# Optimization experiments

Measured on AMD Instinct MI355X. Metric: run time of the kernel, lower is better.

The kernel has to match this reference:

```python
import jax, jax.numpy as jnp
import numpy as np
from jax import lax

H = 1024
W = 1024
WIN = 32
STR = 16
NH = (H - WIN) // STR + 1  # 63
N = NH * NH                # 3969 patches
DN3 = ('NCDHW', 'OIDHW', 'NCDHW')
DN2 = ('NCHW', 'OIHW', 'NCHW')


def setup_inputs() -> dict:
    key = jax.random.key(0)
    ks = jax.random.split(key, 13)
    r = lambda k, s, sc=0.05: jax.random.normal(k, s, dtype=jnp.float32) * sc
    return {
        'x1': jax.random.normal(ks[0], (1, 1, 1, H, W), jnp.float32),
        'x2': jax.random.normal(ks[1], (1, 1, 1, H, W), jnp.float32),
        'conv1_w': r(ks[2], (24, 1, 2, 8, 8)),      # Conv3d(1,24,(2,8,8)) [O,I,D,H,W]
        'conv1_b': r(ks[3], (24,)),
        'conv2_w': r(ks[4], (60, 24, 5, 5)),         # Conv2d(24,60,5)
        'conv2_b': r(ks[5], (60,)),
        'deconv2_w': r(ks[6], (60, 24, 5, 5)),       # ConvTranspose2d(60,24,5) [I,O,kH,kW]
        'deconv2_b': r(ks[7], (24,)),
        'deconv1_w': r(ks[8], (24, 1, 2, 8, 8)),     # ConvTranspose3d(24,1,(2,8,8)) [I,O,D,H,W]
        'deconv1_b': r(ks[9], (1,)),
        'lin_w': r(ks[10], (N, 2), 0.5),             # per-patch Linear(2,1) weights
        'lin_b': r(ks[11], (N,), 0.5),               # per-patch Linear(2,1) bias
        'linear1_w': r(ks[12], (1, 1), 0.5),         # Linear(1,1,bias=False)
    }


def _conv(x, w, b, dn):
    nd = w.ndim - 2
    y = lax.conv_general_dilated(x, w, (1,) * nd, 'VALID', dimension_numbers=dn)
    return y + b.reshape((1, -1) + (1,) * nd)


def _convT(x, w, b, dn):
    # stride-1, pad-0 transposed conv == full-pad conv with flipped, IO-swapped kernel
    nd = w.ndim - 2
    wf = jnp.flip(w, axis=tuple(range(2, w.ndim))).swapaxes(0, 1)  # [O,I,*k]
    pad = [(k - 1, k - 1) for k in w.shape[2:]]
    y = lax.conv_general_dilated(x, wf, (1,) * nd, pad, dimension_numbers=dn)
    return y + b.reshape((1, -1) + (1,) * nd)


def reference(x1, x2, conv1_w, conv1_b, conv2_w, conv2_b, deconv2_w, deconv2_b,
              deconv1_w, deconv1_b, lin_w, lin_b, linear1_w):
    x = jnp.concatenate([x1, x2], axis=2)[0, 0]  # [2,H,W]
    idx = (jnp.arange(NH) * STR)[:, None] + jnp.arange(WIN)[None, :]  # [NH,32]
    # unfold dims 3,4 with window 32 / stride 16 -> [2,NH,NW,32,32]
    patches = x[:, idx[:, None, :, None], idx[None, :, None, :]]
    outX = patches.reshape(2, N, WIN, WIN).transpose(1, 0, 2, 3)[:, None]  # [N,1,2,32,32]
    h = jax.nn.elu(_conv(outX, conv1_w, conv1_b, DN3))        # [N,24,1,25,25]
    h = jax.nn.relu(_conv(h[:, :, 0], conv2_w, conv2_b, DN2))  # [N,60,21,21]
    h = jax.nn.elu(_convT(h, deconv2_w, deconv2_b, DN2))       # [N,24,25,25]
    h = _convT(h[:, :, None], deconv1_w, deconv1_b, DN3)       # [N,1,2,32,32]
    # per-patch Linear(2,1) over depth channels, batched over all patches
    p = jnp.einsum('nchw,nc->nhw', h[:, 0], lin_w) + lin_b[:, None, None]  # [N,32,32]
    p = p.reshape(NH, NH, WIN, WIN)
    # col2im: overlap-add fold, block 32, stride 16 -> [H,W]
    recon = jnp.zeros((H, W), jnp.float32).at[idx[:, None, :, None], idx[None, :, None, :]].add(p)
    outX2 = recon * linear1_w[0, 0]  # Linear(1,1,bias=False) per pixel
    return x2 - outX2.reshape(x2.shape)
```

## Files before the change

kernel.cpp:

```cpp
#include <hip/hip_runtime.h>
#include <hip/hip_bf16.h>

static constexpr int H_ = 1024;
static constexpr int W_ = 1024;
static constexpr int STR_ = 16;
static constexpr int NH_ = 63;
static constexpr int NPATCH_ = NH_ * NH_;
static constexpr int NGRP_ = 32;
static constexpr int NBLK_ = NH_ * NGRP_;

typedef short bf16x8 __attribute__((ext_vector_type(8)));
typedef short short4v __attribute__((ext_vector_type(4)));
typedef float f32x4 __attribute__((ext_vector_type(4)));

static constexpr int GAP16   = 49200;
static constexpr int CP0     = 49216;
static constexpr int CP1     = 55360;
static constexpr int SH2_0   = 49216;
static constexpr int SH2SZ   = 52920;
static constexpr int SH2_1   = SH2_0 + SH2SZ;
static constexpr int ZROW    = 155056;
static constexpr int H3SZ    = 30000;
static constexpr int SWC0    = 60000;
static constexpr int SWC1    = 64096;
static constexpr int SPA     = 68192;
static constexpr int LDS_BYTES = 155200;

__device__ __forceinline__ unsigned short f2bf(float x) {
    __hip_bfloat16 b = __float2bfloat16(x);
    return __builtin_bit_cast(unsigned short, b);
}

__device__ __forceinline__ f32x4 mfma_bf16(bf16x8 a, bf16x8 b, f32x4 c) {
    return __builtin_amdgcn_mfma_f32_16x16x32_bf16(a, b, c, 0, 0, 0);
}

__device__ __forceinline__ float elu_neg(float x) { return __expf(x) - 1.f; }

__global__
__attribute__((amdgpu_flat_work_group_size(1024, 1024), amdgpu_waves_per_eu(4, 4)))
void fused_patch_kernel(
    const float* __restrict__ x1, const float* __restrict__ x2,
    const float* __restrict__ c1b, const float* __restrict__ c2b,
    const float* __restrict__ d2b, const float* __restrict__ d1b,
    const float* __restrict__ lin_w, const float* __restrict__ lin_b,
    const unsigned short* __restrict__ w1frag,
    const unsigned short* __restrict__ w2frag,
    const unsigned short* __restrict__ dw2frag,
    const float* __restrict__ dw1,
    float* __restrict__ recon)
{
    __shared__ alignas(16) char sbuf[LDS_BYTES];
    const int b   = blockIdx.x;
    const int pi  = b / NGRP_, g = b - pi * NGRP_;
    const int pj0 = 2 * g;
    const int npat = (pj0 + 1 < NH_) ? 2 : 1;
    const int n0  = pi * NH_ + pj0;
    const int n1  = (npat == 2) ? (n0 + 1) : n0;
    const int Y0  = pi * STR_, X0 = pj0 * STR_;
    const int t   = (int)threadIdx.x;
    const int wv  = t >> 6, lane = t & 63;
    const int ln15 = lane & 15, quad = lane >> 4;

    bf16x8 w1b[8];
    #pragma unroll
    for (int gg = 0; gg < 8; ++gg)
        w1b[gg] = *(const bf16x8*)(w1frag + (gg * 64 + lane) * 8);
    const float lw00 = lin_w[2 * n0], lw01 = lin_w[2 * n0 + 1];
    const float lw10 = lin_w[2 * n1], lw11 = lin_w[2 * n1 + 1];
    const float lbn0 = lin_b[n0], lbn1 = lin_b[n1];
    const float d1b0 = d1b[0];
    const f32x4 c1bq0 = *(const f32x4*)(c1b + quad * 4);
    f32x4 c1bq1 = (f32x4){0.f, 0.f, 0.f, 0.f};
    if (quad < 2) c1bq1 = *(const f32x4*)(c1b + 16 + quad * 4);
    const f32x4 d2bq0 = *(const f32x4*)(d2b + quad * 4);
    f32x4 d2bq1 = (f32x4){0.f, 0.f, 0.f, 0.f};
    if (quad < 2) d2bq1 = *(const f32x4*)(d2b + 16 + quad * 4);
    float dwp[4] = {0.f, 0.f, 0.f, 0.f};
    {
        int r0 = t >> 5, c0 = t & 31;
        if (c0 < 24) {
            dwp[0] = dw1[(c0 * 2 + 0) * 64 + r0];
            dwp[1] = dw1[(c0 * 2 + 1) * 64 + r0];
        }
        int k1 = t + 1024, r1 = k1 >> 5, c1 = k1 & 31;
        if (c1 < 24) {
            dwp[2] = dw1[(c1 * 2 + 0) * 64 + r1];
            dwp[3] = dw1[(c1 * 2 + 1) * 64 + r1];
        }
    }

    if (t < 4)       ((float*)(sbuf + GAP16))[t] = 0.f;
    else if (t < 8)  ((float*)(sbuf + SH2_1))[t - 4] = 0.f;
    else if (t < 42) ((float*)(sbuf + ZROW))[t - 8] = 0.f;
    #pragma unroll
    for (int it = 0; it < 3; ++it) {
        int k = t + it * 1024;
        int d = (k >= 1536) ? 1 : 0;
        int rem = k - d * 1536;
        int y = rem / 48, x = rem - y * 48;
        int xg = X0 + x; if (xg > W_ - 1) xg = W_ - 1;
        unsigned short bb = f2bf((d ? x2 : x1)[(Y0 + y) * W_ + xg]);
        int row = (d * 32 + y) * 48;
        ((unsigned short*)(sbuf + CP0))[row + x] = bb;
        if (x > 0) ((unsigned short*)(sbuf + CP1))[row + x - 1] = bb;
    }
    __syncthreads();

    for (int tl = wv; tl < 65; tl += 16) {
        const int rawm = tl * 16 + ln15;
        int m = rawm; if (m > 1024) m = 1024;
        int u = m / 41, v = m - u * 41;
        const char* cps = sbuf + ((v & 1) ? CP1 : CP0);
        const int vb2 = (v & ~1) * 2;
        f32x4 acc[2];
        acc[0] = (f32x4){0.f, 0.f, 0.f, 0.f};
        acc[1] = (f32x4){0.f, 0.f, 0.f, 0.f};
        #pragma unroll
        for (int kc = 0; kc < 4; ++kc) {
            const int idx8 = kc * 4 + quad;
            const int dd = idx8 >> 3, pp = idx8 & 7;
            const unsigned int* ap = (const unsigned int*)(cps + (dd * 32 + u + pp) * 96 + vb2);
            union { unsigned int u4[4]; bf16x8 v8; } af;
            af.u4[0] = ap[0]; af.u4[1] = ap[1]; af.u4[2] = ap[2]; af.u4[3] = ap[3];
            acc[0] = mfma_bf16(w1b[kc * 2 + 0], af.v8, acc[0]);
            acc[1] = mfma_bf16(w1b[kc * 2 + 1], af.v8, acc[1]);
        }
        if (rawm < 1025) {
            char* rowp = sbuf + rawm * 48;
            short4v p0;
            #pragma unroll
            for (int r = 0; r < 4; ++r) {
                float hv = acc[0][r] + c1bq0[r];
                hv = hv > 0.f ? hv : elu_neg(hv);
                p0[r] = (short)f2bf(hv);
            }
            *(short4v*)(rowp + quad * 8) = p0;
            if (quad < 2) {
                short4v p1;
                #pragma unroll
                for (int r = 0; r < 4; ++r) {
                    float hw = acc[1][r] + c1bq1[r];
                    hw = hw > 0.f ? hw : elu_neg(hw);
                    p1[r] = (short)f2bf(hw);
                }
                *(short4v*)(rowp + 32 + quad * 8) = p1;
            }
        }
    }
    __syncthreads();

    auto s2pass = [&](int t0, int t1) {
        const bool h1 = (t1 < 56);
        int ab[2], loc[2], Pp[2];
        #pragma unroll
        for (int i = 0; i < 2; ++i) {
            int tt = i ? (h1 ? t1 : t0) : t0;
            int P = (tt >= 28) ? 1 : 0;
            int lc = tt - P * 28;
            int mm = lc * 16 + ln15; if (mm > 440) mm = 440;
            int y = mm / 21, x = mm - y * 21;
            ab[i] = (y * 41 + P * 16 + x) * 48;
            loc[i] = lc; Pp[i] = P;
        }
        f32x4 acc2[2][4];
        #pragma unroll
        for (int i = 0; i < 2; ++i)
            #pragma unroll
            for (int nt = 0; nt < 4; ++nt)
                acc2[i][nt] = (f32x4){0.f, 0.f, 0.f, 0.f};
        const unsigned short* wb = w2frag + lane * 8;
        #pragma unroll
        for (int p = 0; p < 5; ++p) {
            #pragma unroll
            for (int q = 0; q < 5; ++q) {
                const int tap  = p * 5 + q;
                const int toff = (p * 41 + q) * 48;
                bf16x8 bfr[4];
                #pragma unroll
                for (int nt = 0; nt < 4; ++nt)
                    bfr[nt] = *(const bf16x8*)(wb + (tap * 4 + nt) * 512);
                {
                    bf16x8 a = *(const bf16x8*)(sbuf + ab[0] + toff + quad * 16);
                    #pragma unroll
                    for (int nt = 0; nt < 4; ++nt)
                        acc2[0][nt] = mfma_bf16(bfr[nt], a, acc2[0][nt]);
                }
                if (h1) {
                    bf16x8 a = *(const bf16x8*)(sbuf + ab[1] + toff + quad * 16);
                    #pragma unroll
                    for (int nt = 0; nt < 4; ++nt)
                        acc2[1][nt] = mfma_bf16(bfr[nt], a, acc2[1][nt]);
                }
            }
        }
        #pragma unroll
        for (int i = 0; i < 2; ++i) {
            if (i == 1 && !h1) continue;
            int rawpix = loc[i] * 16 + ln15;
            if (rawpix < 441) {
                char* rowp = sbuf + SH2_0 + Pp[i] * SH2SZ + rawpix * 120;
                #pragma unroll
                for (int nt = 0; nt < 4; ++nt) {
                    if (nt == 3 && quad == 3) continue;
                    const f32x4 bq = *(const f32x4*)(c2b + nt * 16 + quad * 4);
                    short4v pk;
                    #pragma unroll
                    for (int r = 0; r < 4; ++r)
                        pk[r] = (short)f2bf(fmaxf(acc2[i][nt][r] + bq[r], 0.f));
                    *(short4v*)(rowp + nt * 32 + quad * 8) = pk;
                }
            }
        }
    };
    s2pass(wv, wv + 16);
    s2pass(wv + 32, wv + 48);
    __syncthreads();

    f32x4 acc3[5][2];
    {
        #pragma unroll
        for (int i = 0; i < 5; ++i) {
            acc3[i][0] = (f32x4){0.f, 0.f, 0.f, 0.f};
            acc3[i][1] = (f32x4){0.f, 0.f, 0.f, 0.f};
        }
        int uarr[5], varr[5], aoff[5];
        bool mval[5];
        #pragma unroll
        for (int i = 0; i < 5; ++i) {
            int t5 = wv + 16 * i;
            int P = (t5 >= 40) ? 1 : 0;
            int lc = t5 - P * 40;
            int m = lc * 16 + ln15;
            mval[i] = (m < 625);
            int mc = mval[i] ? m : 0;
            uarr[i] = mc / 25; varr[i] = mc - uarr[i] * 25;
            aoff[i] = SH2_0 + P * SH2SZ + (uarr[i] * 21 + varr[i]) * 120;
        }
        const unsigned short* db = dw2frag + lane * 8;
        #pragma unroll
        for (int dy = 0; dy < 5; ++dy) {
            #pragma unroll
            for (int dx = 0; dx < 5; ++dx) {
                const int tap = dy * 5 + dx;
                const int t2o = (dy * 21 + dx) * 120;
                bf16x8 bc0 = *(const bf16x8*)(db + tap * 2048);
                bf16x8 bc1 = *(const bf16x8*)(db + tap * 2048 + 512);
                bf16x8 bc2 = *(const bf16x8*)(db + tap * 2048 + 1024);
                bf16x8 bc3 = *(const bf16x8*)(db + tap * 2048 + 1536);
                #pragma unroll
                for (int i = 0; i < 5; ++i) {
                    int yv = uarr[i] - dy, xv = varr[i] - dx;
                    bool ok = mval[i] && ((unsigned)yv < 21u) && ((unsigned)xv < 21u);
                    int ra = ok ? (aoff[i] - t2o) : ZROW;
                    const char* ap = sbuf + ra + quad * 16;
                    short4v lo0 = *(const short4v*)(ap);
                    short4v hi0 = *(const short4v*)(ap + 8);
                    bf16x8 a0 = __builtin_shufflevector(lo0, hi0, 0, 1, 2, 3, 4, 5, 6, 7);
                    acc3[i][0] = mfma_bf16(bc0, a0, acc3[i][0]);
                    acc3[i][1] = mfma_bf16(bc1, a0, acc3[i][1]);
                    short4v lo1 = *(const short4v*)(ap + 64);
                    short4v hi1 = *(const short4v*)(ap + 72);
                    bf16x8 a1 = __builtin_shufflevector(lo1, hi1, 0, 1, 2, 3, 4, 5, 6, 7);
                    acc3[i][0] = mfma_bf16(bc2, a1, acc3[i][0]);
                    acc3[i][1] = mfma_bf16(bc3, a1, acc3[i][1]);
                }
            }
        }
    }
    __syncthreads();

    float* sp = (float*)(sbuf + SPA);
    {
        #pragma unroll
        for (int i = 0; i < 5; ++i) {
            int t5 = wv + 16 * i;
            int P = (t5 >= 40) ? 1 : 0;
            int lc = t5 - P * 40;
            int pix = lc * 16 + ln15;
            if (pix < 625) {
                char* rowp = sbuf + P * H3SZ + pix * 48;
                short4v p0;
                #pragma unroll
                for (int r = 0; r < 4; ++r) {
                    float hv = acc3[i][0][r] + d2bq0[r];
                    hv = hv > 0.f ? hv : elu_neg(hv);
                    p0[r] = (short)f2bf(hv);
                }
                *(short4v*)(rowp + quad * 8) = p0;
                if (quad < 2) {
                    short4v p1;
                    #pragma unroll
                    for (int r = 0; r < 4; ++r) {
                        float hw = acc3[i][1][r] + d2bq1[r];
                        hw = hw > 0.f ? hw : elu_neg(hw);
                        p1[r] = (short)f2bf(hw);
                    }
                    *(short4v*)(rowp + 32 + quad * 8) = p1;
                }
            }
        }
    }
    {
        int r0 = t >> 5, c0 = t & 31;
        ((unsigned short*)(sbuf + SWC0))[r0 * 32 + c0] = f2bf(lw00 * dwp[0] + lw01 * dwp[1]);
        ((unsigned short*)(sbuf + SWC1))[r0 * 32 + c0] = f2bf(lw10 * dwp[0] + lw11 * dwp[1]);
        int k1 = t + 1024, r1 = k1 >> 5, c1 = k1 & 31;
        ((unsigned short*)(sbuf + SWC0))[r1 * 32 + c1] = f2bf(lw00 * dwp[2] + lw01 * dwp[3]);
        ((unsigned short*)(sbuf + SWC1))[r1 * 32 + c1] = f2bf(lw10 * dwp[2] + lw11 * dwp[3]);
    }
    sp[t] = 0.f; sp[t + 1024] = 0.f;
    __syncthreads();

    {
        int qoff[4];
        #pragma unroll
        for (int r = 0; r < 4; ++r) {
            int qr = quad * 4 + r;
            qoff[r] = (qr >> 3) * 32 + (qr & 7);
        }
        #pragma unroll
        for (int i = 0; i < 5; ++i) {
            int t5 = wv + 16 * i;
            int P = (t5 >= 40) ? 1 : 0;
            int lc = t5 - P * 40;
            int rawpix = lc * 16 + ln15;
            bool pok = (rawpix < 625);
            int pc = pok ? rawpix : 624;
            bf16x8 a = *(const bf16x8*)(sbuf + P * H3SZ + pc * 48 + quad * 16);
            const char* swc = sbuf + (P ? SWC1 : SWC0);
            float* spP = sp + P * 1024;
            int uvbase = (pc / 25) * 32 + (pc % 25);
            #pragma unroll
            for (int nt = 0; nt < 4; ++nt) {
                bf16x8 wbv = *(const bf16x8*)(swc + (nt * 16 + ln15) * 64 + quad * 16);
                f32x4 acc4 = (f32x4){0.f, 0.f, 0.f, 0.f};
                acc4 = mfma_bf16(wbv, a, acc4);
                if (pok) {
                    #pragma unroll
                    for (int r = 0; r < 4; ++r)
                        atomicAdd(&spP[uvbase + nt * 64 + qoff[r]], acc4[r]);
                }
            }
        }
    }
    __syncthreads();

    {
        int yy = t >> 5, xx = t & 31;
        float ob0 = d1b0 * (lw00 + lw01) + lbn0;
        atomicAdd(&recon[(Y0 + yy) * W_ + X0 + xx], sp[t] + ob0);
        if (npat == 2) {
            float ob1 = d1b0 * (lw10 + lw11) + lbn1;
            atomicAdd(&recon[(Y0 + yy) * W_ + X0 + 16 + xx], sp[t + 1024] + ob1);
        }
    }
}

__global__ void prep_kernel(const float* __restrict__ c1w,
                            const float* __restrict__ c2w,
                            const float* __restrict__ d2w,
                            unsigned short* __restrict__ w1frag,
                            unsigned short* __restrict__ w2frag,
                            unsigned short* __restrict__ dw2frag)
{
    int i = blockIdx.x * blockDim.x + threadIdx.x;
    if (i < 51200) {
        int j = i & 7, lane = (i >> 3) & 63;
        int ln15 = lane & 15, quad = lane >> 4;
        if (i < 4096) {
            int g = i >> 9;
            int kc = g >> 1, nt = g & 1;
            int nn = nt * 16 + ln15, k = kc * 32 + quad * 8 + j;
            w1frag[i] = f2bf((nn < 24) ? c1w[nn * 128 + k] : 0.f);
        }
        {
            int nt = (i >> 9) & 3, tap = i >> 11;
            int o = nt * 16 + ln15, c = quad * 8 + j;
            float v = (o < 60 && c < 24) ? c2w[(o * 24 + c) * 25 + tap] : 0.f;
            w2frag[i] = f2bf(v);
        }
        {
            int nt = (i >> 9) & 1, kc = (i >> 10) & 1, tap = i >> 11;
            int k = kc * 32 + quad * 8 + j, c = nt * 16 + ln15;
            float v = (k < 60 && c < 24) ? d2w[(k * 24 + c) * 25 + tap] : 0.f;
            dw2frag[i] = f2bf(v);
        }
    }
}

__global__ void finalize_kernel(const float* __restrict__ x2,
                                const float* __restrict__ l1w,
                                float* __restrict__ out)
{
    int i = blockIdx.x * blockDim.x + threadIdx.x;
    if (i < H_ * W_) {
        float r = out[i];
        out[i] = x2[i] - r * l1w[0];
    }
}

extern "C" void kernel_launch(void* const* d_in, const int* in_sizes, int n_in,
                              void* d_out, int out_size, void* d_ws, size_t ws_size,
                              hipStream_t stream)
{
    const float* x1  = (const float*)d_in[0];
    const float* x2  = (const float*)d_in[1];
    const float* c1w = (const float*)d_in[2];
    const float* c1b = (const float*)d_in[3];
    const float* c2w = (const float*)d_in[4];
    const float* c2b = (const float*)d_in[5];
    const float* d2w = (const float*)d_in[6];
    const float* d2b = (const float*)d_in[7];
    const float* d1w = (const float*)d_in[8];
    const float* d1b = (const float*)d_in[9];
    const float* lw  = (const float*)d_in[10];
    const float* lb  = (const float*)d_in[11];
    const float* l1w = (const float*)d_in[12];

    float*          out     = (float*)d_out;
    unsigned short* w1frag  = (unsigned short*)d_ws;
    unsigned short* w2frag  = (unsigned short*)((char*)d_ws + 8192);
    unsigned short* dw2frag = (unsigned short*)((char*)d_ws + 110592);

    hipMemsetAsync(d_out, 0, (size_t)H_ * W_ * sizeof(float), stream);
    prep_kernel<<<100, 512, 0, stream>>>(c1w, c2w, d2w, w1frag, w2frag, dw2frag);
    fused_patch_kernel<<<NBLK_, 1024, 0, stream>>>(x1, x2, c1b, c2b, d2b, d1b,
                                                   lw, lb, w1frag, w2frag, dw2frag,
                                                   d1w, out);
    finalize_kernel<<<(H_ * W_ + 255) / 256, 256, 0, stream>>>(x2, l1w, out);
}
```

Measured before the change: 1.338 ms.

## Split fused patch kernel into per-stage kernels with global intermediates

Replaces the single fused kernel with four per-patch kernels: conv1, conv2, deconv2 and epilogue. The fused kernel processes two patches per block with 1024 threads and about 155KB of LDS. The new kernels pass bf16 activations through workspace buffers in global memory. Smaller LDS footprints and smaller blocks should allow more resident blocks per CU and less barrier stalling. In exchange it adds hundreds of MB of global write/read traffic and four launches, and it loses the conv1 input sharing between adjacent patches. The split path runs only when the workspace is large enough; otherwise the fused kernel is used.

```diff
diff --git a/kernel.cpp b/kernel.cpp
--- a/kernel.cpp
+++ b/kernel.cpp
@@ -6,25 +6,17 @@
 static constexpr int STR_ = 16;
 static constexpr int NH_ = 63;
 static constexpr int NPATCH_ = NH_ * NH_;
-static constexpr int NGRP_ = 32;
-static constexpr int NBLK_ = NH_ * NGRP_;
 
 typedef short bf16x8 __attribute__((ext_vector_type(8)));
 typedef short short4v __attribute__((ext_vector_type(4)));
 typedef float f32x4 __attribute__((ext_vector_type(4)));
 
-static constexpr int GAP16   = 49200;
-static constexpr int CP0     = 49216;
-static constexpr int CP1     = 55360;
-static constexpr int SH2_0   = 49216;
-static constexpr int SH2SZ   = 52920;
-static constexpr int SH2_1   = SH2_0 + SH2SZ;
-static constexpr int ZROW    = 155056;
-static constexpr int H3SZ    = 30000;
-static constexpr int SWC0    = 60000;
-static constexpr int SWC1    = 64096;
-static constexpr int SPA     = 68192;
-static constexpr int LDS_BYTES = 155200;
+static constexpr size_t FRAG_BYTES = 212992;
+static constexpr size_t H1_SLAB    = 30768;
+static constexpr size_t H2_SLAB    = 53248;
+static constexpr size_t H1_BYTES   = (size_t)NPATCH_ * H1_SLAB;
+static constexpr size_t H2_BYTES   = (size_t)NPATCH_ * H2_SLAB;
+static constexpr size_t WS_NEED    = FRAG_BYTES + H1_BYTES + H2_BYTES;
 
 __device__ __forceinline__ unsigned short f2bf(float x) {
     __hip_bfloat16 b = __float2bfloat16(x);
@@ -36,6 +28,298 @@
 }
 
 __device__ __forceinline__ float elu_neg(float x) { return __expf(x) - 1.f; }
+
+__global__ __launch_bounds__(256) void k_conv1(
+    const float* __restrict__ x1, const float* __restrict__ x2,
+    const float* __restrict__ c1b, const unsigned short* __restrict__ w1frag,
+    unsigned short* __restrict__ h1)
+{
+    __shared__ alignas(16) char sbuf[10240];
+    const int n = blockIdx.x, t = (int)threadIdx.x;
+    const int pi = n / NH_, pj = n % NH_;
+    const int Y0 = pi * STR_, X0 = pj * STR_;
+    const int wv = t >> 6, lane = t & 63;
+    const int ln15 = lane & 15, quad = lane >> 4;
+    unsigned short* h1n = h1 + (size_t)n * (H1_SLAB / 2);
+
+    bf16x8 w1b[8];
+    #pragma unroll
+    for (int g = 0; g < 8; ++g)
+        w1b[g] = *(const bf16x8*)(w1frag + (g * 64 + lane) * 8);
+    const f32x4 c1bq0 = *(const f32x4*)(c1b + quad * 4);
+    f32x4 c1bq1 = (f32x4){0.f, 0.f, 0.f, 0.f};
+    if (quad < 2) c1bq1 = *(const f32x4*)(c1b + 16 + quad * 4);
+
+    if (t < 6) ((unsigned long long*)(h1n + 625 * 24))[t] = 0ull;
+
+    for (int k = t; k < 2048; k += 256) {
+        int d = k >> 10, r = k & 1023, y = r >> 5, x = r & 31;
+        unsigned short bb = f2bf((d ? x2 : x1)[(Y0 + y) * W_ + (X0 + x)]);
+        int row = (d * 32 + y) * 40;
+        ((unsigned short*)(sbuf))[row + x] = bb;
+        if (x > 0) ((unsigned short*)(sbuf + 5120))[row + x - 1] = bb;
+    }
+    __syncthreads();
+
+    for (int tl = wv; tl < 40; tl += 4) {
+        const int rawm = tl * 16 + ln15;
+        int m = rawm > 624 ? 624 : rawm;
+        int u = m / 25, v = m - u * 25;
+        const char* cps = sbuf + ((v & 1) ? 5120 : 0);
+        const int vb2 = (v & ~1) * 2;
+        f32x4 acc0 = (f32x4){0.f, 0.f, 0.f, 0.f};
+        f32x4 acc1 = (f32x4){0.f, 0.f, 0.f, 0.f};
+        #pragma unroll
+        for (int kc = 0; kc < 4; ++kc) {
+            const int idx8 = kc * 4 + quad;
+            const int dd = idx8 >> 3, pp = idx8 & 7;
+            const unsigned int* ap = (const unsigned int*)(cps + (dd * 32 + u + pp) * 80 + vb2);
+            union { unsigned int u4[4]; bf16x8 v8; } af;
+            af.u4[0] = ap[0]; af.u4[1] = ap[1]; af.u4[2] = ap[2]; af.u4[3] = ap[3];
+            acc0 = mfma_bf16(w1b[kc * 2 + 0], af.v8, acc0);
+            acc1 = mfma_bf16(w1b[kc * 2 + 1], af.v8, acc1);
+        }
+        if (rawm < 625) {
+            unsigned short* rowp = h1n + rawm * 24;
+            short4v p0;
+            #pragma unroll
+            for (int r = 0; r < 4; ++r) {
+                float hv = acc0[r] + c1bq0[r];
+                hv = hv > 0.f ? hv : elu_neg(hv);
+                p0[r] = (short)f2bf(hv);
+            }
+            *(short4v*)(rowp + quad * 4) = p0;
+            if (quad < 2) {
+                short4v p1;
+                #pragma unroll
+                for (int r = 0; r < 4; ++r) {
+                    float hw = acc1[r] + c1bq1[r];
+                    hw = hw > 0.f ? hw : elu_neg(hw);
+                    p1[r] = (short)f2bf(hw);
+                }
+                *(short4v*)(rowp + 16 + quad * 4) = p1;
+            }
+        }
+    }
+}
+
+__global__ __launch_bounds__(256) void k_conv2(
+    const float* __restrict__ c2b, const unsigned short* __restrict__ w2frag,
+    const unsigned short* __restrict__ h1, unsigned short* __restrict__ h2)
+{
+    __shared__ alignas(16) char sbuf[30048];
+    const int n = blockIdx.x, t = (int)threadIdx.x;
+    const int wv = t >> 6, lane = t & 63;
+    const int ln15 = lane & 15, quad = lane >> 4;
+    {
+        const f32x4* src = (const f32x4*)(h1 + (size_t)n * (H1_SLAB / 2));
+        f32x4* dst = (f32x4*)sbuf;
+        for (int i = t; i < 1878; i += 256) dst[i] = src[i];
+    }
+    __syncthreads();
+
+    const unsigned short* wb = w2frag + lane * 8;
+    unsigned short* h2n = h2 + (size_t)n * (H2_SLAB / 2);
+
+    for (int mt = wv; mt < 28; mt += 4) {
+        int mm = mt * 16 + ln15; if (mm > 440) mm = 440;
+        int y = mm / 21, x = mm - y * 21;
+        const int abase = (y * 25 + x) * 48;
+        f32x4 acc[4];
+        #pragma unroll
+        for (int nt = 0; nt < 4; ++nt) acc[nt] = (f32x4){0.f, 0.f, 0.f, 0.f};
+        #pragma unroll
+        for (int p = 0; p < 5; ++p) {
+            #pragma unroll
+            for (int q = 0; q < 5; ++q) {
+                const int tap  = p * 5 + q;
+                const int toff = (p * 25 + q) * 48;
+                bf16x8 bfr[4];
+                #pragma unroll
+                for (int nt = 0; nt < 4; ++nt)
+                    bfr[nt] = *(const bf16x8*)(wb + (tap * 4 + nt) * 512);
+                bf16x8 a = *(const bf16x8*)(sbuf + abase + toff + quad * 16);
+                #pragma unroll
+                for (int nt = 0; nt < 4; ++nt)
+                    acc[nt] = mfma_bf16(bfr[nt], a, acc[nt]);
+            }
+        }
+        int rawpix = mt * 16 + ln15;
+        if (rawpix < 441) {
+            unsigned short* rowp = h2n + rawpix * 60;
+            #pragma unroll
+            for (int nt = 0; nt < 4; ++nt) {
+                if (nt == 3 && quad == 3) continue;
+                const f32x4 bq = *(const f32x4*)(c2b + nt * 16 + quad * 4);
+                short4v pk;
+                #pragma unroll
+                for (int r = 0; r < 4; ++r)
+                    pk[r] = (short)f2bf(fmaxf(acc[nt][r] + bq[r], 0.f));
+                *(short4v*)(rowp + nt * 16 + quad * 4) = pk;
+            }
+        }
+    }
+}
+
+__global__ __launch_bounds__(512) void k_deconv2(
+    const float* __restrict__ d2b, const unsigned short* __restrict__ dw2frag,
+    const unsigned short* __restrict__ h2, unsigned short* __restrict__ h3)
+{
+    __shared__ alignas(16) char sbuf[53056];
+    const int n = blockIdx.x, t = (int)threadIdx.x;
+    const int wv = t >> 6, lane = t & 63;
+    const int ln15 = lane & 15, quad = lane >> 4;
+    {
+        const f32x4* src = (const f32x4*)(h2 + (size_t)n * (H2_SLAB / 2));
+        f32x4* dst = (f32x4*)sbuf;
+        for (int i = t; i < 3307; i += 512) dst[i] = src[i];
+        if (t == 0)
+            *(unsigned long long*)(sbuf + 52912) =
+                *(const unsigned long long*)((const char*)src + 52912);
+        if (t >= 64 && t < 81)
+            ((unsigned long long*)(sbuf + 52920))[t - 64] = 0ull;
+    }
+    __syncthreads();
+
+    const unsigned short* db = dw2frag + lane * 8;
+    const f32x4 d2bq0 = *(const f32x4*)(d2b + quad * 4);
+    f32x4 d2bq1 = (f32x4){0.f, 0.f, 0.f, 0.f};
+    if (quad < 2) d2bq1 = *(const f32x4*)(d2b + 16 + quad * 4);
+    unsigned short* h3n = h3 + (size_t)n * (H1_SLAB / 2);
+
+    for (int mt = wv; mt < 40; mt += 8) {
+        const int m = mt * 16 + ln15;
+        const bool mv = (m < 625);
+        const int mc = mv ? m : 0;
+        const int ua = mc / 25, va = mc - ua * 25;
+        const int aoff = (ua * 21 + va) * 120;
+        f32x4 accN0 = (f32x4){0.f, 0.f, 0.f, 0.f};
+        f32x4 accN1 = (f32x4){0.f, 0.f, 0.f, 0.f};
+        #pragma unroll
+        for (int dy = 0; dy < 5; ++dy) {
+            #pragma unroll
+            for (int dx = 0; dx < 5; ++dx) {
+                const int tap = dy * 5 + dx;
+                const int t2o = (dy * 21 + dx) * 120;
+                bf16x8 bc0 = *(const bf16x8*)(db + tap * 2048);
+                bf16x8 bc1 = *(const bf16x8*)(db + tap * 2048 + 512);
+                bf16x8 bc2 = *(const bf16x8*)(db + tap * 2048 + 1024);
+                bf16x8 bc3 = *(const bf16x8*)(db + tap * 2048 + 1536);
+                int yv = ua - dy, xv = va - dx;
+                bool ok = mv && ((unsigned)yv < 21u) && ((unsigned)xv < 21u);
+                int ra = ok ? (aoff - t2o) : 52920;
+                const char* ap = sbuf + ra + quad * 16;
+                short4v lo0 = *(const short4v*)(ap);
+                short4v hi0 = *(const short4v*)(ap + 8);
+                bf16x8 a0 = __builtin_shufflevector(lo0, hi0, 0, 1, 2, 3, 4, 5, 6, 7);
+                accN0 = mfma_bf16(bc0, a0, accN0);
+                accN1 = mfma_bf16(bc1, a0, accN1);
+                short4v lo1 = *(const short4v*)(ap + 64);
+                short4v hi1 = *(const short4v*)(ap + 72);
+                bf16x8 a1 = __builtin_shufflevector(lo1, hi1, 0, 1, 2, 3, 4, 5, 6, 7);
+                accN0 = mfma_bf16(bc2, a1, accN0);
+                accN1 = mfma_bf16(bc3, a1, accN1);
+            }
+        }
+        if (m < 625) {
+            unsigned short* rowp = h3n + m * 24;
+            short4v p0;
+            #pragma unroll
+            for (int r = 0; r < 4; ++r) {
+                float hv = accN0[r] + d2bq0[r];
+                hv = hv > 0.f ? hv : elu_neg(hv);
+                p0[r] = (short)f2bf(hv);
+            }
+            *(short4v*)(rowp + quad * 4) = p0;
+            if (quad < 2) {
+                short4v p1;
+                #pragma unroll
+                for (int r = 0; r < 4; ++r) {
+                    float hw = accN1[r] + d2bq1[r];
+                    hw = hw > 0.f ? hw : elu_neg(hw);
+                    p1[r] = (short)f2bf(hw);
+                }
+                *(short4v*)(rowp + 16 + quad * 4) = p1;
+            }
+        }
+    }
+}
+
+__global__ __launch_bounds__(256) void k_epilogue(
+    const float* __restrict__ d1b, const float* __restrict__ lin_w,
+    const float* __restrict__ lin_b, const float* __restrict__ dw1,
+    const unsigned short* __restrict__ h3, float* __restrict__ recon)
+{
+    __shared__ alignas(16) char sbuf[38240];
+    const int n = blockIdx.x, t = (int)threadIdx.x;
+    const int pi = n / NH_, pj = n % NH_;
+    const int Y0 = pi * STR_, X0 = pj * STR_;
+    const int wv = t >> 6, lane = t & 63;
+    const int ln15 = lane & 15, quad = lane >> 4;
+    const float lw0 = lin_w[2 * n], lw1 = lin_w[2 * n + 1];
+    {
+        const f32x4* src = (const f32x4*)(h3 + (size_t)n * (H1_SLAB / 2));
+        f32x4* dst = (f32x4*)sbuf;
+        for (int i = t; i < 1878; i += 256) dst[i] = src[i];
+    }
+    unsigned short* swc = (unsigned short*)(sbuf + 30048);
+    float* sp = (float*)(sbuf + 34144);
+    for (int k = t; k < 2048; k += 256) {
+        int r = k >> 5, c = k & 31;
+        float v = 0.f;
+        if (c < 24)
+            v = lw0 * dw1[(c * 2 + 0) * 64 + r] + lw1 * dw1[(c * 2 + 1) * 64 + r];
+        swc[r * 32 + c] = f2bf(v);
+    }
+    for (int k = t; k < 1024; k += 256) sp[k] = 0.f;
+    __syncthreads();
+
+    int qoff[4];
+    #pragma unroll
+    for (int r = 0; r < 4; ++r) {
+        int qr = quad * 4 + r;
+        qoff[r] = (qr >> 3) * 32 + (qr & 7);
+    }
+    for (int mt = wv; mt < 40; mt += 4) {
+        int rawpix = mt * 16 + ln15;
+        bool pok = (rawpix < 625);
+        int pc = pok ? rawpix : 624;
+        bf16x8 a = *(const bf16x8*)(sbuf + pc * 48 + quad * 16);
+        int uvbase = (pc / 25) * 32 + (pc % 25);
+        #pragma unroll
+        for (int nt = 0; nt < 4; ++nt) {
+            bf16x8 wbv = *(const bf16x8*)((char*)swc + (nt * 16 + ln15) * 64 + quad * 16);
+            f32x4 a4 = (f32x4){0.f, 0.f, 0.f, 0.f};
+            a4 = mfma_bf16(wbv, a, a4);
+            if (pok) {
+                #pragma unroll
+                for (int r = 0; r < 4; ++r)
+                    atomicAdd(&sp[uvbase + nt * 64 + qoff[r]], a4[r]);
+            }
+        }
+    }
+    __syncthreads();
+    const float obias = d1b[0] * (lw0 + lw1) + lin_b[n];
+    for (int k = t; k < 1024; k += 256) {
+        int yy = k >> 5, xx = k & 31;
+        atomicAdd(&recon[(Y0 + yy) * W_ + (X0 + xx)], sp[k] + obias);
+    }
+}
+
+static constexpr int FGAP16 = 49200;
+static constexpr int FCP0   = 49216;
+static constexpr int FCP1   = 55360;
+static constexpr int FSH2_0 = 49216;
+static constexpr int FSH2SZ = 52920;
+static constexpr int FSH2_1 = FSH2_0 + FSH2SZ;
+static constexpr int FZROW  = 155056;
+static constexpr int FH3SZ  = 30000;
+static constexpr int FSWC0  = 60000;
+static constexpr int FSWC1  = 64096;
+static constexpr int FSPA   = 68192;
+static constexpr int FLDS   = 155200;
+static constexpr int FNGRP  = 32;
+static constexpr int FNBLK  = NH_ * FNGRP;
 
 __global__
 __attribute__((amdgpu_flat_work_group_size(1024, 1024), amdgpu_waves_per_eu(4, 4)))
@@ -50,9 +334,9 @@
     const float* __restrict__ dw1,
     float* __restrict__ recon)
 {
-    __shared__ alignas(16) char sbuf[LDS_BYTES];
+    __shared__ alignas(16) char sbuf[FLDS];
     const int b   = blockIdx.x;
-    const int pi  = b / NGRP_, g = b - pi * NGRP_;
+    const int pi  = b / FNGRP, g = b - pi * FNGRP;
     const int pj0 = 2 * g;
     const int npat = (pj0 + 1 < NH_) ? 2 : 1;
     const int n0  = pi * NH_ + pj0;
@@ -90,9 +374,9 @@
         }
     }
 
-    if (t < 4)       ((float*)(sbuf + GAP16))[t] = 0.f;
-    else if (t < 8)  ((float*)(sbuf + SH2_1))[t - 4] = 0.f;
-    else if (t < 42) ((float*)(sbuf + ZROW))[t - 8] = 0.f;
+    if (t < 4)       ((float*)(sbuf + FGAP16))[t] = 0.f;
+    else if (t < 8)  ((float*)(sbuf + FSH2_1))[t - 4] = 0.f;
+    else if (t < 42) ((float*)(sbuf + FZROW))[t - 8] = 0.f;
     #pragma unroll
     for (int it = 0; it < 3; ++it) {
         int k = t + it * 1024;
@@ -102,8 +386,8 @@
         int xg = X0 + x; if (xg > W_ - 1) xg = W_ - 1;
         unsigned short bb = f2bf((d ? x2 : x1)[(Y0 + y) * W_ + xg]);
         int row = (d * 32 + y) * 48;
-        ((unsigned short*)(sbuf + CP0))[row + x] = bb;
-        if (x > 0) ((unsigned short*)(sbuf + CP1))[row + x - 1] = bb;
+        ((unsigned short*)(sbuf + FCP0))[row + x] = bb;
+        if (x > 0) ((unsigned short*)(sbuf + FCP1))[row + x - 1] = bb;
     }
     __syncthreads();
 
@@ -111,7 +395,7 @@
         const int rawm = tl * 16 + ln15;
         int m = rawm; if (m > 1024) m = 1024;
         int u = m / 41, v = m - u * 41;
-        const char* cps = sbuf + ((v & 1) ? CP1 : CP0);
+        const char* cps = sbuf + ((v & 1) ? FCP1 : FCP0);
         const int vb2 = (v & ~1) * 2;
         f32x4 acc[2];
         acc[0] = (f32x4){0.f, 0.f, 0.f, 0.f};
@@ -151,11 +435,11 @@
     __syncthreads();
 
     auto s2pass = [&](int t0, int t1) {
-        const bool h1 = (t1 < 56);
+        const bool h1ok = (t1 < 56);
         int ab[2], loc[2], Pp[2];
         #pragma unroll
         for (int i = 0; i < 2; ++i) {
-            int tt = i ? (h1 ? t1 : t0) : t0;
+            int tt = i ? (h1ok ? t1 : t0) : t0;
             int P = (tt >= 28) ? 1 : 0;
             int lc = tt - P * 28;
             int mm = lc * 16 + ln15; if (mm > 440) mm = 440;
@@ -186,7 +470,7 @@
                     for (int nt = 0; nt < 4; ++nt)
                         acc2[0][nt] = mfma_bf16(bfr[nt], a, acc2[0][nt]);
                 }
-                if (h1) {
+                if (h1ok) {
                     bf16x8 a = *(const bf16x8*)(sbuf + ab[1] + toff + quad * 16);
                     #pragma unroll
                     for (int nt = 0; nt < 4; ++nt)
@@ -196,10 +480,10 @@
         }
         #pragma unroll
         for (int i = 0; i < 2; ++i) {
-            if (i == 1 && !h1) continue;
+            if (i == 1 && !h1ok) continue;
             int rawpix = loc[i] * 16 + ln15;
             if (rawpix < 441) {
-                char* rowp = sbuf + SH2_0 + Pp[i] * SH2SZ + rawpix * 120;
+                char* rowp = sbuf + FSH2_0 + Pp[i] * FSH2SZ + rawpix * 120;
                 #pragma unroll
                 for (int nt = 0; nt < 4; ++nt) {
                     if (nt == 3 && quad == 3) continue;
@@ -235,7 +519,7 @@
             mval[i] = (m < 625);
             int mc = mval[i] ? m : 0;
             uarr[i] = mc / 25; varr[i] = mc - uarr[i] * 25;
-            aoff[i] = SH2_0 + P * SH2SZ + (uarr[i] * 21 + varr[i]) * 120;
+            aoff[i] = FSH2_0 + P * FSH2SZ + (uarr[i] * 21 + varr[i]) * 120;
         }
         const unsigned short* db = dw2frag + lane * 8;
         #pragma unroll
@@ -252,7 +536,7 @@
                 for (int i = 0; i < 5; ++i) {
                     int yv = uarr[i] - dy, xv = varr[i] - dx;
                     bool ok = mval[i] && ((unsigned)yv < 21u) && ((unsigned)xv < 21u);
-                    int ra = ok ? (aoff[i] - t2o) : ZROW;
+                    int ra = ok ? (aoff[i] - t2o) : FZROW;
                     const char* ap = sbuf + ra + quad * 16;
                     short4v lo0 = *(const short4v*)(ap);
                     short4v hi0 = *(const short4v*)(ap + 8);
@@ -270,7 +554,7 @@
     }
     __syncthreads();
 
-    float* sp = (float*)(sbuf + SPA);
+    float* sp = (float*)(sbuf + FSPA);
     {
         #pragma unroll
         for (int i = 0; i < 5; ++i) {
@@ -279,7 +563,7 @@
             int lc = t5 - P * 40;
             int pix = lc * 16 + ln15;
             if (pix < 625) {
-                char* rowp = sbuf + P * H3SZ + pix * 48;
+                char* rowp = sbuf + P * FH3SZ + pix * 48;
                 short4v p0;
                 #pragma unroll
                 for (int r = 0; r < 4; ++r) {
@@ -303,11 +587,11 @@
     }
     {
         int r0 = t >> 5, c0 = t & 31;
-        ((unsigned short*)(sbuf + SWC0))[r0 * 32 + c0] = f2bf(lw00 * dwp[0] + lw01 * dwp[1]);
-        ((unsigned short*)(sbuf + SWC1))[r0 * 32 + c0] = f2bf(lw10 * dwp[0] + lw11 * dwp[1]);
+        ((unsigned short*)(sbuf + FSWC0))[r0 * 32 + c0] = f2bf(lw00 * dwp[0] + lw01 * dwp[1]);
+        ((unsigned short*)(sbuf + FSWC1))[r0 * 32 + c0] = f2bf(lw10 * dwp[0] + lw11 * dwp[1]);
         int k1 = t + 1024, r1 = k1 >> 5, c1 = k1 & 31;
-        ((unsigned short*)(sbuf + SWC0))[r1 * 32 + c1] = f2bf(lw00 * dwp[2] + lw01 * dwp[3]);
-        ((unsigned short*)(sbuf + SWC1))[r1 * 32 + c1] = f2bf(lw10 * dwp[2] + lw11 * dwp[3]);
+        ((unsigned short*)(sbuf + FSWC0))[r1 * 32 + c1] = f2bf(lw00 * dwp[2] + lw01 * dwp[3]);
+        ((unsigned short*)(sbuf + FSWC1))[r1 * 32 + c1] = f2bf(lw10 * dwp[2] + lw11 * dwp[3]);
     }
     sp[t] = 0.f; sp[t + 1024] = 0.f;
     __syncthreads();
@@ -327,8 +611,8 @@
             int rawpix = lc * 16 + ln15;
             bool pok = (rawpix < 625);
             int pc = pok ? rawpix : 624;
-            bf16x8 a = *(const bf16x8*)(sbuf + P * H3SZ + pc * 48 + quad * 16);
-            const char* swc = sbuf + (P ? SWC1 : SWC0);
+            bf16x8 a = *(const bf16x8*)(sbuf + P * FH3SZ + pc * 48 + quad * 16);
+            const char* swc = sbuf + (P ? FSWC1 : FSWC0);
             float* spP = sp + P * 1024;
             int uvbase = (pc / 25) * 32 + (pc % 25);
             #pragma unroll
@@ -425,8 +709,19 @@
 
     hipMemsetAsync(d_out, 0, (size_t)H_ * W_ * sizeof(float), stream);
     prep_kernel<<<100, 512, 0, stream>>>(c1w, c2w, d2w, w1frag, w2frag, dw2frag);
-    fused_patch_kernel<<<NBLK_, 1024, 0, stream>>>(x1, x2, c1b, c2b, d2b, d1b,
-                                                   lw, lb, w1frag, w2frag, dw2frag,
-                                                   d1w, out);
+
+    if (ws_size >= WS_NEED) {
+        unsigned short* h1 = (unsigned short*)((char*)d_ws + FRAG_BYTES);
+        unsigned short* h2 = (unsigned short*)((char*)d_ws + FRAG_BYTES + H1_BYTES);
+        unsigned short* h3 = h1;
+        k_conv1<<<NPATCH_, 256, 0, stream>>>(x1, x2, c1b, w1frag, h1);
+        k_conv2<<<NPATCH_, 256, 0, stream>>>(c2b, w2frag, h1, h2);
+        k_deconv2<<<NPATCH_, 512, 0, stream>>>(d2b, dw2frag, h2, h3);
+        k_epilogue<<<NPATCH_, 256, 0, stream>>>(d1b, lw, lb, d1w, h3, out);
+    } else {
+        fused_patch_kernel<<<FNBLK, 1024, 0, stream>>>(x1, x2, c1b, c2b, d2b, d1b,
+                                                       lw, lb, w1frag, w2frag, dw2frag,
+                                                       d1w, out);
+    }
     finalize_kernel<<<(H_ * W_ + 255) / 256, 256, 0, stream>>>(x2, l1w, out);
 }
```

Result: no change. 1.340 ms (+0.2%).

## Use 32x32x16 MFMA for deconv2 stage with XOR-swizzled padded LDS rows

Applied to the files above, without the earlier changes.

The deconv2 (transposed 5x5 conv) stage switches from 16x16x32 MFMAs with 16-pixel tiles to 32x32x16 MFMAs with 32-pixel tiles. The conv2 output rows in LDS are padded from 120 to 128 bytes and XOR-swizzled to avoid bank conflicts on the new 16-byte reads. The deconv2 weight fragments are repacked to match the new layout. This cuts instruction count and the split short4 loads, at the cost of more LDS (which may limit occupancy) and some idle waves in the third tile.

```diff
diff --git a/kernel.cpp b/kernel.cpp
--- a/kernel.cpp
+++ b/kernel.cpp
@@ -6,25 +6,26 @@
 static constexpr int STR_ = 16;
 static constexpr int NH_ = 63;
 static constexpr int NPATCH_ = NH_ * NH_;
-static constexpr int NGRP_ = 32;
-static constexpr int NBLK_ = NH_ * NGRP_;
 
 typedef short bf16x8 __attribute__((ext_vector_type(8)));
 typedef short short4v __attribute__((ext_vector_type(4)));
 typedef float f32x4 __attribute__((ext_vector_type(4)));
-
-static constexpr int GAP16   = 49200;
-static constexpr int CP0     = 49216;
-static constexpr int CP1     = 55360;
-static constexpr int SH2_0   = 49216;
-static constexpr int SH2SZ   = 52920;
-static constexpr int SH2_1   = SH2_0 + SH2SZ;
-static constexpr int ZROW    = 155056;
-static constexpr int H3SZ    = 30000;
-static constexpr int SWC0    = 60000;
-static constexpr int SWC1    = 64096;
-static constexpr int SPA     = 68192;
-static constexpr int LDS_BYTES = 155200;
+typedef float f32x16 __attribute__((ext_vector_type(16)));
+
+static constexpr int FGAP16 = 49200;
+static constexpr int FCP0   = 49280;
+static constexpr int FCP1   = 55424;
+static constexpr int FSH2_0 = 49280;
+static constexpr int FSH2SZ = 56448;
+static constexpr int FSH2_1 = FSH2_0 + FSH2SZ;
+static constexpr int FZROW  = 162176;
+static constexpr int FH3SZ  = 30000;
+static constexpr int FSWC0  = 60000;
+static constexpr int FSWC1  = 64096;
+static constexpr int FSPA   = 68192;
+static constexpr int FLDS   = 162320;
+static constexpr int FNGRP  = 32;
+static constexpr int FNBLK  = NH_ * FNGRP;
 
 __device__ __forceinline__ unsigned short f2bf(float x) {
     __hip_bfloat16 b = __float2bfloat16(x);
@@ -33,6 +34,10 @@
 
 __device__ __forceinline__ f32x4 mfma_bf16(bf16x8 a, bf16x8 b, f32x4 c) {
     return __builtin_amdgcn_mfma_f32_16x16x32_bf16(a, b, c, 0, 0, 0);
+}
+
+__device__ __forceinline__ f32x16 mfma32_bf16(bf16x8 a, bf16x8 b, f32x16 c) {
+    return __builtin_amdgcn_mfma_f32_32x32x16_bf16(a, b, c, 0, 0, 0);
 }
 
 __device__ __forceinline__ float elu_neg(float x) { return __expf(x) - 1.f; }
@@ -50,9 +55,9 @@
     const float* __restrict__ dw1,
     float* __restrict__ recon)
 {
-    __shared__ alignas(16) char sbuf[LDS_BYTES];
+    __shared__ alignas(16) char sbuf[FLDS];
     const int b   = blockIdx.x;
-    const int pi  = b / NGRP_, g = b - pi * NGRP_;
+    const int pi  = b / FNGRP, g = b - pi * FNGRP;
     const int pj0 = 2 * g;
     const int npat = (pj0 + 1 < NH_) ? 2 : 1;
     const int n0  = pi * NH_ + pj0;
@@ -73,9 +78,6 @@
     const f32x4 c1bq0 = *(const f32x4*)(c1b + quad * 4);
     f32x4 c1bq1 = (f32x4){0.f, 0.f, 0.f, 0.f};
     if (quad < 2) c1bq1 = *(const f32x4*)(c1b + 16 + quad * 4);
-    const f32x4 d2bq0 = *(const f32x4*)(d2b + quad * 4);
-    f32x4 d2bq1 = (f32x4){0.f, 0.f, 0.f, 0.f};
-    if (quad < 2) d2bq1 = *(const f32x4*)(d2b + 16 + quad * 4);
     float dwp[4] = {0.f, 0.f, 0.f, 0.f};
     {
         int r0 = t >> 5, c0 = t & 31;
@@ -90,9 +92,9 @@
         }
     }
 
-    if (t < 4)       ((float*)(sbuf + GAP16))[t] = 0.f;
-    else if (t < 8)  ((float*)(sbuf + SH2_1))[t - 4] = 0.f;
-    else if (t < 42) ((float*)(sbuf + ZROW))[t - 8] = 0.f;
+    if (t < 4)       ((float*)(sbuf + FGAP16))[t] = 0.f;
+    else if (t < 8)  ((float*)(sbuf + FSH2_1))[t - 4] = 0.f;
+    else if (t < 42) ((float*)(sbuf + FZROW))[t - 8] = 0.f;
     #pragma unroll
     for (int it = 0; it < 3; ++it) {
         int k = t + it * 1024;
@@ -102,8 +104,8 @@
         int xg = X0 + x; if (xg > W_ - 1) xg = W_ - 1;
         unsigned short bb = f2bf((d ? x2 : x1)[(Y0 + y) * W_ + xg]);
         int row = (d * 32 + y) * 48;
-        ((unsigned short*)(sbuf + CP0))[row + x] = bb;
-        if (x > 0) ((unsigned short*)(sbuf + CP1))[row + x - 1] = bb;
+        ((unsigned short*)(sbuf + FCP0))[row + x] = bb;
+        if (x > 0) ((unsigned short*)(sbuf + FCP1))[row + x - 1] = bb;
     }
     __syncthreads();
 
@@ -111,7 +113,7 @@
         const int rawm = tl * 16 + ln15;
         int m = rawm; if (m > 1024) m = 1024;
         int u = m / 41, v = m - u * 41;
-        const char* cps = sbuf + ((v & 1) ? CP1 : CP0);
+        const char* cps = sbuf + ((v & 1) ? FCP1 : FCP0);
         const int vb2 = (v & ~1) * 2;
         f32x4 acc[2];
         acc[0] = (f32x4){0.f, 0.f, 0.f, 0.f};
@@ -151,11 +153,11 @@
     __syncthreads();
 
     auto s2pass = [&](int t0, int t1) {
-        const bool h1 = (t1 < 56);
+        const bool h1ok = (t1 < 56);
         int ab[2], loc[2], Pp[2];
         #pragma unroll
         for (int i = 0; i < 2; ++i) {
-            int tt = i ? (h1 ? t1 : t0) : t0;
+            int tt = i ? (h1ok ? t1 : t0) : t0;
             int P = (tt >= 28) ? 1 : 0;
             int lc = tt - P * 28;
             int mm = lc * 16 + ln15; if (mm > 440) mm = 440;
@@ -186,7 +188,7 @@
                     for (int nt = 0; nt < 4; ++nt)
                         acc2[0][nt] = mfma_bf16(bfr[nt], a, acc2[0][nt]);
                 }
-                if (h1) {
+                if (h1ok) {
                     bf16x8 a = *(const bf16x8*)(sbuf + ab[1] + toff + quad * 16);
                     #pragma unroll
                     for (int nt = 0; nt < 4; ++nt)
@@ -196,19 +198,25 @@
         }
         #pragma unroll
         for (int i = 0; i < 2; ++i) {
-            if (i == 1 && !h1) continue;
+            if (i == 1 && !h1ok) continue;
             int rawpix = loc[i] * 16 + ln15;
             if (rawpix < 441) {
-                char* rowp = sbuf + SH2_0 + Pp[i] * SH2SZ + rawpix * 120;
+                const int rowbyte = FSH2_0 + Pp[i] * FSH2SZ + rawpix * 128;
+                char* rowp = sbuf + rowbyte;
+                const int sw = ((rowbyte >> 7) & 7) << 4;
                 #pragma unroll
                 for (int nt = 0; nt < 4; ++nt) {
-                    if (nt == 3 && quad == 3) continue;
-                    const f32x4 bq = *(const f32x4*)(c2b + nt * 16 + quad * 4);
-                    short4v pk;
-                    #pragma unroll
-                    for (int r = 0; r < 4; ++r)
-                        pk[r] = (short)f2bf(fmaxf(acc2[i][nt][r] + bq[r], 0.f));
-                    *(short4v*)(rowp + nt * 32 + quad * 8) = pk;
+                    const int goff = nt * 32 + quad * 8;
+                    if (nt == 3 && quad == 3) {
+                        *(short4v*)(rowp + (goff ^ sw)) = (short4v){0, 0, 0, 0};
+                    } else {
+                        const f32x4 bq = *(const f32x4*)(c2b + nt * 16 + quad * 4);
+                        short4v pk;
+                        #pragma unroll
+                        for (int r = 0; r < 4; ++r)
+                            pk[r] = (short)f2bf(fmaxf(acc2[i][nt][r] + bq[r], 0.f));
+                        *(short4v*)(rowp + (goff ^ sw)) = pk;
+                    }
                 }
             }
         }
@@ -217,97 +225,95 @@
     s2pass(wv + 32, wv + 48);
     __syncthreads();
 
-    f32x4 acc3[5][2];
-    {
-        #pragma unroll
-        for (int i = 0; i < 5; ++i) {
-            acc3[i][0] = (f32x4){0.f, 0.f, 0.f, 0.f};
-            acc3[i][1] = (f32x4){0.f, 0.f, 0.f, 0.f};
-        }
-        int uarr[5], varr[5], aoff[5];
-        bool mval[5];
-        #pragma unroll
-        for (int i = 0; i < 5; ++i) {
+    f32x16 acc3[3];
+    {
+        #pragma unroll
+        for (int i = 0; i < 3; ++i)
+            #pragma unroll
+            for (int r = 0; r < 16; ++r) acc3[i][r] = 0.f;
+
+        int uarr[3], varr[3], aoff[3];
+        bool mval[3];
+        #pragma unroll
+        for (int i = 0; i < 3; ++i) {
             int t5 = wv + 16 * i;
-            int P = (t5 >= 40) ? 1 : 0;
-            int lc = t5 - P * 40;
-            int m = lc * 16 + ln15;
+            int P = (t5 >= 20) ? 1 : 0;
+            int lc = t5 - P * 20;
+            int m = lc * 32 + (lane & 31);
             mval[i] = (m < 625);
             int mc = mval[i] ? m : 0;
             uarr[i] = mc / 25; varr[i] = mc - uarr[i] * 25;
-            aoff[i] = SH2_0 + P * SH2SZ + (uarr[i] * 21 + varr[i]) * 120;
+            aoff[i] = FSH2_0 + P * FSH2SZ + (uarr[i] * 21 + varr[i]) * 128;
         }
         const unsigned short* db = dw2frag + lane * 8;
+        const int hh16 = (lane >> 5) * 16;
         #pragma unroll
         for (int dy = 0; dy < 5; ++dy) {
             #pragma unroll
             for (int dx = 0; dx < 5; ++dx) {
                 const int tap = dy * 5 + dx;
-                const int t2o = (dy * 21 + dx) * 120;
-                bf16x8 bc0 = *(const bf16x8*)(db + tap * 2048);
-                bf16x8 bc1 = *(const bf16x8*)(db + tap * 2048 + 512);
-                bf16x8 bc2 = *(const bf16x8*)(db + tap * 2048 + 1024);
-                bf16x8 bc3 = *(const bf16x8*)(db + tap * 2048 + 1536);
+                const int t2o = (dy * 21 + dx) * 128;
+                bf16x8 bw0 = *(const bf16x8*)(db + tap * 2048);
+                bf16x8 bw1 = *(const bf16x8*)(db + tap * 2048 + 512);
+                bf16x8 bw2 = *(const bf16x8*)(db + tap * 2048 + 1024);
+                bf16x8 bw3 = *(const bf16x8*)(db + tap * 2048 + 1536);
                 #pragma unroll
-                for (int i = 0; i < 5; ++i) {
+                for (int i = 0; i < 3; ++i) {
+                    if (i == 2 && wv >= 8) continue;
                     int yv = uarr[i] - dy, xv = varr[i] - dx;
                     bool ok = mval[i] && ((unsigned)yv < 21u) && ((unsigned)xv < 21u);
-                    int ra = ok ? (aoff[i] - t2o) : ZROW;
-                    const char* ap = sbuf + ra + quad * 16;
-                    short4v lo0 = *(const short4v*)(ap);
-                    short4v hi0 = *(const short4v*)(ap + 8);
-                    bf16x8 a0 = __builtin_shufflevector(lo0, hi0, 0, 1, 2, 3, 4, 5, 6, 7);
-                    acc3[i][0] = mfma_bf16(bc0, a0, acc3[i][0]);
-                    acc3[i][1] = mfma_bf16(bc1, a0, acc3[i][1]);
-                    short4v lo1 = *(const short4v*)(ap + 64);
-                    short4v hi1 = *(const short4v*)(ap + 72);
-                    bf16x8 a1 = __builtin_shufflevector(lo1, hi1, 0, 1, 2, 3, 4, 5, 6, 7);
-                    acc3[i][0] = mfma_bf16(bc2, a1, acc3[i][0]);
-                    acc3[i][1] = mfma_bf16(bc3, a1, acc3[i][1]);
-                }
-            }
-        }
-    }
-    __syncthreads();
-
-    float* sp = (float*)(sbuf + SPA);
-    {
-        #pragma unroll
-        for (int i = 0; i < 5; ++i) {
+                    int ra = ok ? (aoff[i] - t2o) : FZROW;
+                    const int s = ((ra >> 7) & 7) << 4;
+                    const char* bp = sbuf + ra;
+                    bf16x8 a0 = *(const bf16x8*)(bp + ((0 + hh16) ^ s));
+                    acc3[i] = mfma32_bf16(bw0, a0, acc3[i]);
+                    bf16x8 a1 = *(const bf16x8*)(bp + ((32 + hh16) ^ s));
+                    acc3[i] = mfma32_bf16(bw1, a1, acc3[i]);
+                    bf16x8 a2 = *(const bf16x8*)(bp + ((64 + hh16) ^ s));
+                    acc3[i] = mfma32_bf16(bw2, a2, acc3[i]);
+                    bf16x8 a3 = *(const bf16x8*)(bp + ((96 + hh16) ^ s));
+                    acc3[i] = mfma32_bf16(bw3, a3, acc3[i]);
+                }
+            }
+        }
+    }
+    __syncthreads();
+
+    float* sp = (float*)(sbuf + FSPA);
+    {
+        const int hh = lane >> 5;
+        #pragma unroll
+        for (int i = 0; i < 3; ++i) {
+            if (i == 2 && wv >= 8) continue;
             int t5 = wv + 16 * i;
-            int P = (t5 >= 40) ? 1 : 0;
-            int lc = t5 - P * 40;
-            int pix = lc * 16 + ln15;
-            if (pix < 625) {
-                char* rowp = sbuf + P * H3SZ + pix * 48;
-                short4v p0;
+            int P = (t5 >= 20) ? 1 : 0;
+            int lc = t5 - P * 20;
+            int p = lc * 32 + (lane & 31);
+            if (p < 625) {
+                char* rowp = sbuf + P * FH3SZ + p * 48;
                 #pragma unroll
-                for (int r = 0; r < 4; ++r) {
-                    float hv = acc3[i][0][r] + d2bq0[r];
-                    hv = hv > 0.f ? hv : elu_neg(hv);
-                    p0[r] = (short)f2bf(hv);
-                }
-                *(short4v*)(rowp + quad * 8) = p0;
-                if (quad < 2) {
-                    short4v p1;
+                for (int gg2 = 0; gg2 < 3; ++gg2) {
+                    const int c0 = gg2 * 8 + hh * 4;
+                    const f32x4 bq = *(const f32x4*)(d2b + c0);
+                    short4v pk;
                     #pragma unroll
                     for (int r = 0; r < 4; ++r) {
-                        float hw = acc3[i][1][r] + d2bq1[r];
-                        hw = hw > 0.f ? hw : elu_neg(hw);
-                        p1[r] = (short)f2bf(hw);
+                        float hv = acc3[i][gg2 * 4 + r] + bq[r];
+                        hv = hv > 0.f ? hv : elu_neg(hv);
+                        pk[r] = (short)f2bf(hv);
                     }
-                    *(short4v*)(rowp + 32 + quad * 8) = p1;
+                    *(short4v*)(rowp + c0 * 2) = pk;
                 }
             }
         }
     }
     {
         int r0 = t >> 5, c0 = t & 31;
-        ((unsigned short*)(sbuf + SWC0))[r0 * 32 + c0] = f2bf(lw00 * dwp[0] + lw01 * dwp[1]);
-        ((unsigned short*)(sbuf + SWC1))[r0 * 32 + c0] = f2bf(lw10 * dwp[0] + lw11 * dwp[1]);
+        ((unsigned short*)(sbuf + FSWC0))[r0 * 32 + c0] = f2bf(lw00 * dwp[0] + lw01 * dwp[1]);
+        ((unsigned short*)(sbuf + FSWC1))[r0 * 32 + c0] = f2bf(lw10 * dwp[0] + lw11 * dwp[1]);
         int k1 = t + 1024, r1 = k1 >> 5, c1 = k1 & 31;
-        ((unsigned short*)(sbuf + SWC0))[r1 * 32 + c1] = f2bf(lw00 * dwp[2] + lw01 * dwp[3]);
-        ((unsigned short*)(sbuf + SWC1))[r1 * 32 + c1] = f2bf(lw10 * dwp[2] + lw11 * dwp[3]);
+        ((unsigned short*)(sbuf + FSWC0))[r1 * 32 + c1] = f2bf(lw00 * dwp[2] + lw01 * dwp[3]);
+        ((unsigned short*)(sbuf + FSWC1))[r1 * 32 + c1] = f2bf(lw10 * dwp[2] + lw11 * dwp[3]);
     }
     sp[t] = 0.f; sp[t + 1024] = 0.f;
     __syncthreads();
@@ -327,8 +333,8 @@
             int rawpix = lc * 16 + ln15;
             bool pok = (rawpix < 625);
             int pc = pok ? rawpix : 624;
-            bf16x8 a = *(const bf16x8*)(sbuf + P * H3SZ + pc * 48 + quad * 16);
-            const char* swc = sbuf + (P ? SWC1 : SWC0);
+            bf16x8 a = *(const bf16x8*)(sbuf + P * FH3SZ + pc * 48 + quad * 16);
+            const char* swc = sbuf + (P ? FSWC1 : FSWC0);
             float* spP = sp + P * 1024;
             int uvbase = (pc / 25) * 32 + (pc % 25);
             #pragma unroll
@@ -381,8 +387,8 @@
             w2frag[i] = f2bf(v);
         }
         {
-            int nt = (i >> 9) & 1, kc = (i >> 10) & 1, tap = i >> 11;
-            int k = kc * 32 + quad * 8 + j, c = nt * 16 + ln15;
+            int ks = (i >> 9) & 3, tap = i >> 11;
+            int k = ks * 16 + (lane >> 5) * 8 + j, c = lane & 31;
             float v = (k < 60 && c < 24) ? d2w[(k * 24 + c) * 25 + tap] : 0.f;
             dw2frag[i] = f2bf(v);
         }
@@ -425,7 +431,7 @@
 
     hipMemsetAsync(d_out, 0, (size_t)H_ * W_ * sizeof(float), stream);
     prep_kernel<<<100, 512, 0, stream>>>(c1w, c2w, d2w, w1frag, w2frag, dw2frag);
-    fused_patch_kernel<<<NBLK_, 1024, 0, stream>>>(x1, x2, c1b, c2b, d2b, d1b,
+    fused_patch_kernel<<<FNBLK, 1024, 0, stream>>>(x1, x2, c1b, c2b, d2b, d1b,
                                                    lw, lb, w1frag, w2frag, dw2frag,
                                                    d1w, out);
     finalize_kernel<<<(H_ * W_ + 255) / 256, 256, 0, stream>>>(x2, l1w, out);
```

Result: no change. 1.343 ms (+0.4%).
